# Kernel tuning notes

Measured on AMD Instinct MI355X. Metric: run time of the kernel, lower is better.

Reference implementation:

```python
import jax, jax.numpy as jnp
import numpy as np

B, C, H, W = 8, 256, 64, 64
NUM_HEADS = 4


def setup_inputs() -> dict:
    key = jax.random.key(0)
    ks = jax.random.split(key, 6)
    s = 0.02  # small init scale for 1x1 conv weights
    return {
        "x": jax.random.normal(ks[0], (B, C, H, W), jnp.float32),
        "cproj": jax.random.normal(ks[1], (B, C, H, W), jnp.float32),
        "wq": jax.random.normal(ks[2], (C, C), jnp.float32) * s,
        "bq": jnp.zeros((C,), jnp.float32),
        "wkv": jax.random.normal(ks[3], (2 * C, C), jnp.float32) * s,
        "bkv": jnp.zeros((2 * C,), jnp.float32),
        "wo": jax.random.normal(ks[4], (C, C), jnp.float32) * s,  # zero_module in torch; random here for a meaningful baseline
        "bo": jnp.zeros((C,), jnp.float32),
    }


def reference(x, cproj, wq, bq, wkv, bkv, wo, bo):
    Bb, Cc, Hh, Ww = x.shape
    N = Hh * Ww
    h = NUM_HEADS
    d = Cc // h
    scale = 1.0 / jnp.sqrt(jnp.sqrt(jnp.asarray(Cc, jnp.float32)))

    xf = x.reshape(Bb, Cc, N)
    cf = cproj.reshape(Bb, Cc, N)

    # 1x1 convs == channel matmuls
    Q = jnp.einsum('oc,bcn->bon', wq, xf) + bq[None, :, None]           # (B,C,N)
    KV = jnp.einsum('oc,bcn->bon', wkv, cf) + bkv[None, :, None]        # (B,2C,N)
    K, V = KV[:, :Cc], KV[:, Cc:]

    # softmax over channel-dim-within-head for q, over spatial N for k
    q = jax.nn.softmax(Q.reshape(Bb, h, d, N) * scale, axis=2).reshape(Bb, Cc, N)
    k = jax.nn.softmax(K.reshape(Bb, h, d, N), axis=3).reshape(Bb, Cc, N)

    # linear-attention: (B,C,C) context, then project back to N — note heads are mixed, per original bmm
    context = jnp.einsum('bcn,bdn->bcd', k, V)
    out = jnp.einsum('bcd,bdn->bcn', context, q)

    out = jnp.einsum('oc,bcn->bon', wo, out) + bo[None, :, None]
    return out.reshape(Bb, Cc, Hh, Ww)
```

## Files before the change

### kernel.cpp

```cpp
#include <hip/hip_runtime.h>

#define B_ 8
#define C_ 256
#define N_ 4096
#define H_ 4
#define KVC_ 512
#define NSPLIT 8

typedef float f32x4 __attribute__((ext_vector_type(4)));
typedef __bf16 bf16x8 __attribute__((ext_vector_type(8)));
typedef unsigned short u16x8 __attribute__((ext_vector_type(8)));
typedef unsigned short u16x4 __attribute__((ext_vector_type(4)));

union BU8 { u16x8 u; bf16x8 b; };

__device__ __forceinline__ unsigned short f2bf(float f) {
  unsigned u = __float_as_uint(f);
  u += 0x7fff + ((u >> 16) & 1);
  return (unsigned short)(u >> 16);
}

__device__ __forceinline__ f32x4 mfma16(bf16x8 a, bf16x8 b, f32x4 c) {
  return __builtin_amdgcn_mfma_f32_16x16x32_bf16(a, b, c, 0, 0, 0);
}

__global__ __launch_bounds__(256) void qproj_softmax(
    const float* __restrict__ wq, const float* __restrict__ x,
    const float* __restrict__ bq, unsigned short* __restrict__ qT) {
  __shared__ unsigned short As[256][40];
  __shared__ unsigned short Bs[32][68];
  __shared__ float bql[C_];
  const int b = blockIdx.z;
  const int n0 = blockIdx.x * 64;
  const int tid = threadIdx.x;
  const int lane = tid & 63, w = tid >> 6;
  const float* xb = x + (size_t)b * C_ * N_;

  bql[tid] = bq[tid];

  f32x4 acc[16];
#pragma unroll
  for (int i = 0; i < 16; i++) acc[i] = (f32x4){0.f, 0.f, 0.f, 0.f};

  const int colL = lane & 15, kq = lane >> 4;
  const int ra = tid >> 3, ca = (tid & 7) * 4;
  const int rb = tid >> 4, cb = (tid & 15) * 4;

  float4 pa[8], pb[2];
#pragma unroll
  for (int i = 0; i < 8; i++) pa[i] = *(const float4*)&wq[(i * 32 + ra) * C_ + ca];
#pragma unroll
  for (int i = 0; i < 2; i++) pb[i] = *(const float4*)&xb[(size_t)(i * 16 + rb) * N_ + n0 + cb];

  for (int kt = 0; kt < 8; kt++) {
#pragma unroll
    for (int i = 0; i < 8; i++) {
      float4 v = pa[i];
      *(u16x4*)&As[i * 32 + ra][ca] = (u16x4){f2bf(v.x), f2bf(v.y), f2bf(v.z), f2bf(v.w)};
    }
#pragma unroll
    for (int i = 0; i < 2; i++) {
      float4 v = pb[i];
      *(u16x4*)&Bs[i * 16 + rb][cb] = (u16x4){f2bf(v.x), f2bf(v.y), f2bf(v.z), f2bf(v.w)};
    }
    __syncthreads();
    if (kt < 7) {
      const int kc = (kt + 1) * 32;
#pragma unroll
      for (int i = 0; i < 8; i++) pa[i] = *(const float4*)&wq[(i * 32 + ra) * C_ + kc + ca];
#pragma unroll
      for (int i = 0; i < 2; i++) pb[i] = *(const float4*)&xb[(size_t)(kc + i * 16 + rb) * N_ + n0 + cb];
    }
    BU8 bu;
#pragma unroll
    for (int j = 0; j < 8; j++) bu.u[j] = Bs[kq * 8 + j][w * 16 + colL];
    bf16x8 bf = bu.b;
#pragma unroll
    for (int mt = 0; mt < 16; mt++) {
      bf16x8 af = *(const bf16x8*)&As[mt * 16 + colL][kq * 8];
      acc[mt] = mfma16(af, bf, acc[mt]);
    }
    __syncthreads();
  }

  const int quad = lane >> 4;
  const int n = n0 + w * 16 + colL;
  unsigned short* qbase = qT + ((size_t)b * N_ + n) * C_;
#pragma unroll
  for (int h = 0; h < H_; h++) {
    float v[16];
    float mx = -1e30f;
#pragma unroll
    for (int i = 0; i < 4; i++) {
      int mt = 4 * h + i;
#pragma unroll
      for (int r = 0; r < 4; r++) {
        int m = mt * 16 + quad * 4 + r;
        float val = (acc[mt][r] + bql[m]) * 0.25f;
        v[i * 4 + r] = val;
        mx = fmaxf(mx, val);
      }
    }
    mx = fmaxf(mx, __shfl_xor(mx, 16));
    mx = fmaxf(mx, __shfl_xor(mx, 32));
    float s = 0.f;
#pragma unroll
    for (int j = 0; j < 16; j++) { v[j] = __expf(v[j] - mx); s += v[j]; }
    s += __shfl_xor(s, 16);
    s += __shfl_xor(s, 32);
    float inv = 1.0f / s;
#pragma unroll
    for (int i = 0; i < 4; i++) {
      u16x4 o = (u16x4){f2bf(v[i * 4 + 0] * inv), f2bf(v[i * 4 + 1] * inv),
                        f2bf(v[i * 4 + 2] * inv), f2bf(v[i * 4 + 3] * inv)};
      *(u16x4*)(qbase + (4 * h + i) * 16 + quad * 4) = o;
    }
  }
}

__global__ __launch_bounds__(256) void kvproj(
    const float* __restrict__ wkv, const float* __restrict__ cp,
    const float* __restrict__ bkv, float* __restrict__ Kf,
    unsigned short* __restrict__ Vb) {
  __shared__ unsigned short As[128][40];
  __shared__ unsigned short Bs[32][136];
  const int b = blockIdx.z;
  const int m0 = blockIdx.y * 128, n0 = blockIdx.x * 128;
  const int tid = threadIdx.x, lane = tid & 63, w = tid >> 6;
  const int m0w = (w >> 1) * 64, n0w = (w & 1) * 64;
  const int colL = lane & 15, kq = lane >> 4;
  const float* cpb = cp + (size_t)b * C_ * N_;

  f32x4 acc[4][4];
#pragma unroll
  for (int i = 0; i < 4; i++)
#pragma unroll
    for (int j = 0; j < 4; j++) acc[i][j] = (f32x4){0.f, 0.f, 0.f, 0.f};

  const int ra = tid >> 3, ca = (tid & 7) * 4;
  const int rb = tid >> 5, cb = (tid & 31) * 4;

  float4 pa[4], pb[4];
#pragma unroll
  for (int i = 0; i < 4; i++) pa[i] = *(const float4*)&wkv[(size_t)(m0 + i * 32 + ra) * C_ + ca];
#pragma unroll
  for (int i = 0; i < 4; i++) pb[i] = *(const float4*)&cpb[(size_t)(i * 8 + rb) * N_ + n0 + cb];

  for (int kt = 0; kt < 8; kt++) {
#pragma unroll
    for (int i = 0; i < 4; i++) {
      float4 v = pa[i];
      *(u16x4*)&As[i * 32 + ra][ca] = (u16x4){f2bf(v.x), f2bf(v.y), f2bf(v.z), f2bf(v.w)};
    }
#pragma unroll
    for (int i = 0; i < 4; i++) {
      float4 v = pb[i];
      *(u16x4*)&Bs[i * 8 + rb][cb] = (u16x4){f2bf(v.x), f2bf(v.y), f2bf(v.z), f2bf(v.w)};
    }
    __syncthreads();
    if (kt < 7) {
      const int kc = (kt + 1) * 32;
#pragma unroll
      for (int i = 0; i < 4; i++) pa[i] = *(const float4*)&wkv[(size_t)(m0 + i * 32 + ra) * C_ + kc + ca];
#pragma unroll
      for (int i = 0; i < 4; i++) pb[i] = *(const float4*)&cpb[(size_t)(kc + i * 8 + rb) * N_ + n0 + cb];
    }
    bf16x8 bfr[4];
#pragma unroll
    for (int nt = 0; nt < 4; nt++) {
      BU8 bu;
#pragma unroll
      for (int j = 0; j < 8; j++) bu.u[j] = Bs[kq * 8 + j][n0w + nt * 16 + colL];
      bfr[nt] = bu.b;
    }
#pragma unroll
    for (int mt = 0; mt < 4; mt++) {
      bf16x8 af = *(const bf16x8*)&As[m0w + mt * 16 + colL][kq * 8];
#pragma unroll
      for (int nt = 0; nt < 4; nt++) acc[mt][nt] = mfma16(af, bfr[nt], acc[mt][nt]);
    }
    __syncthreads();
  }

  const int quad = lane >> 4;
#pragma unroll
  for (int mt = 0; mt < 4; mt++) {
#pragma unroll
    for (int r = 0; r < 4; r++) {
      int m = m0 + m0w + mt * 16 + quad * 4 + r;
      float bias = bkv[m];
#pragma unroll
      for (int nt = 0; nt < 4; nt++) {
        int n = n0 + n0w + nt * 16 + colL;
        float val = acc[mt][nt][r] + bias;
        if (m0 < C_) {
          Kf[((size_t)b * C_ + m) * N_ + n] = val;
        } else {
          Vb[((size_t)b * C_ + (m - C_)) * N_ + n] = f2bf(val);
        }
      }
    }
  }
}

__global__ __launch_bounds__(256) void ksoftmax(const float* __restrict__ Kf,
                                                unsigned short* __restrict__ kb) {
  const int b = blockIdx.x >> 8, c = blockIdx.x & 255;
  const float* row = Kf + ((size_t)b * C_ + c) * N_;
  unsigned short* orow = kb + ((size_t)b * C_ + c) * N_;
  const int t = threadIdx.x, lane = t & 63, wv = t >> 6;
  __shared__ float red[8];

  float4 v[4];
  float mx = -1e30f;
#pragma unroll
  for (int i = 0; i < 4; i++) {
    v[i] = *(const float4*)&row[i * 1024 + t * 4];
    mx = fmaxf(fmaxf(fmaxf(mx, v[i].x), fmaxf(v[i].y, v[i].z)), v[i].w);
  }
#pragma unroll
  for (int o = 32; o > 0; o >>= 1) mx = fmaxf(mx, __shfl_down(mx, o));
  if (lane == 0) red[wv] = mx;
  __syncthreads();
  mx = fmaxf(fmaxf(red[0], red[1]), fmaxf(red[2], red[3]));

  float s = 0.f;
#pragma unroll
  for (int i = 0; i < 4; i++) {
    v[i].x = __expf(v[i].x - mx); v[i].y = __expf(v[i].y - mx);
    v[i].z = __expf(v[i].z - mx); v[i].w = __expf(v[i].w - mx);
    s += v[i].x + v[i].y + v[i].z + v[i].w;
  }
#pragma unroll
  for (int o = 32; o > 0; o >>= 1) s += __shfl_down(s, o);
  if (lane == 0) red[4 + wv] = s;
  __syncthreads();
  float inv = 1.0f / (red[4] + red[5] + red[6] + red[7]);
#pragma unroll
  for (int i = 0; i < 4; i++) {
    u16x4 o = (u16x4){f2bf(v[i].x * inv), f2bf(v[i].y * inv),
                      f2bf(v[i].z * inv), f2bf(v[i].w * inv)};
    *(u16x4*)&orow[i * 1024 + t * 4] = o;
  }
}

__global__ __launch_bounds__(256) void ctx_part(
    const unsigned short* __restrict__ kb, const unsigned short* __restrict__ Vb,
    float* __restrict__ ctxp) {
  __shared__ unsigned short As[128][72];
  __shared__ unsigned short Bs[128][72];
  const int z = blockIdx.z, b = z >> 3, s = z & 7;
  const int m0 = blockIdx.y * 128, n0 = blockIdx.x * 128;
  const int tid = threadIdx.x, lane = tid & 63, w = tid >> 6;
  const int m0w = (w >> 1) * 64, n0w = (w & 1) * 64;
  const int colL = lane & 15, kq = lane >> 4;
  const unsigned short* Ab = kb + (size_t)b * C_ * N_;
  const unsigned short* Bb = Vb + (size_t)b * C_ * N_;

  f32x4 acc[4][4];
#pragma unroll
  for (int i = 0; i < 4; i++)
#pragma unroll
    for (int j = 0; j < 4; j++) acc[i][j] = (f32x4){0.f, 0.f, 0.f, 0.f};

  const int rs = tid >> 3, cs = (tid & 7) * 8;
  const int kbeg = s * (N_ / NSPLIT);

  u16x8 pa[4], pb[4];
#pragma unroll
  for (int i = 0; i < 4; i++) {
    pa[i] = *(const u16x8*)&Ab[(size_t)(m0 + i * 32 + rs) * N_ + kbeg + cs];
    pb[i] = *(const u16x8*)&Bb[(size_t)(n0 + i * 32 + rs) * N_ + kbeg + cs];
  }

  for (int kt = 0; kt < (N_ / NSPLIT) / 64; kt++) {
#pragma unroll
    for (int i = 0; i < 4; i++) {
      *(u16x8*)&As[i * 32 + rs][cs] = pa[i];
      *(u16x8*)&Bs[i * 32 + rs][cs] = pb[i];
    }
    __syncthreads();
    if (kt < (N_ / NSPLIT) / 64 - 1) {
      const int kc = kbeg + (kt + 1) * 64;
#pragma unroll
      for (int i = 0; i < 4; i++) {
        pa[i] = *(const u16x8*)&Ab[(size_t)(m0 + i * 32 + rs) * N_ + kc + cs];
        pb[i] = *(const u16x8*)&Bb[(size_t)(n0 + i * 32 + rs) * N_ + kc + cs];
      }
    }
#pragma unroll
    for (int ks = 0; ks < 2; ks++) {
      bf16x8 af[4], bfr[4];
#pragma unroll
      for (int mt = 0; mt < 4; mt++) af[mt] = *(const bf16x8*)&As[m0w + mt * 16 + colL][ks * 32 + kq * 8];
#pragma unroll
      for (int nt = 0; nt < 4; nt++) bfr[nt] = *(const bf16x8*)&Bs[n0w + nt * 16 + colL][ks * 32 + kq * 8];
#pragma unroll
      for (int mt = 0; mt < 4; mt++)
#pragma unroll
        for (int nt = 0; nt < 4; nt++) acc[mt][nt] = mfma16(af[mt], bfr[nt], acc[mt][nt]);
    }
    __syncthreads();
  }

  float* outp = ctxp + ((size_t)s * B_ + b) * C_ * C_;
  const int quad = lane >> 4;
#pragma unroll
  for (int mt = 0; mt < 4; mt++)
#pragma unroll
    for (int nt = 0; nt < 4; nt++)
#pragma unroll
      for (int r = 0; r < 4; r++) {
        int m = m0 + m0w + mt * 16 + quad * 4 + r;
        int n = n0 + n0w + nt * 16 + colL;
        outp[(size_t)m * C_ + n] = acc[mt][nt][r];
      }
}

__global__ __launch_bounds__(256) void ctx_reduce(const float* __restrict__ ctxp,
                                                  unsigned short* __restrict__ ctxs) {
  const size_t e = ((size_t)blockIdx.x * 256 + threadIdx.x) * 4;
  float4 a = {0.f, 0.f, 0.f, 0.f};
#pragma unroll
  for (int s = 0; s < NSPLIT; s++) {
    float4 v = *(const float4*)&ctxp[(size_t)s * B_ * C_ * C_ + e];
    a.x += v.x; a.y += v.y; a.z += v.z; a.w += v.w;
  }
  *(u16x4*)&ctxs[e] = (u16x4){f2bf(a.x), f2bf(a.y), f2bf(a.z), f2bf(a.w)};
}

__global__ __launch_bounds__(256) void oproj(const float* __restrict__ wo,
                                             const unsigned short* __restrict__ ctxs,
                                             unsigned short* __restrict__ ctx2) {
  __shared__ unsigned short As[128][40];
  __shared__ unsigned short Bs[32][136];
  const int b = blockIdx.z;
  const int m0 = blockIdx.y * 128, n0 = blockIdx.x * 128;
  const int tid = threadIdx.x, lane = tid & 63, w = tid >> 6;
  const int m0w = (w >> 1) * 64, n0w = (w & 1) * 64;
  const int colL = lane & 15, kq = lane >> 4;
  const unsigned short* cb = ctxs + (size_t)b * C_ * C_;

  f32x4 acc[4][4];
#pragma unroll
  for (int i = 0; i < 4; i++)
#pragma unroll
    for (int j = 0; j < 4; j++) acc[i][j] = (f32x4){0.f, 0.f, 0.f, 0.f};

  for (int kc = 0; kc < C_; kc += 32) {
    __syncthreads();
#pragma unroll
    for (int i = 0; i < 4; i++) {
      int r = i * 32 + (tid >> 3), c = (tid & 7) * 4;
      float4 v = *(const float4*)&wo[(size_t)(m0 + r) * C_ + kc + c];
      *(u16x4*)&As[r][c] = (u16x4){f2bf(v.x), f2bf(v.y), f2bf(v.z), f2bf(v.w)};
    }
#pragma unroll
    for (int i = 0; i < 2; i++) {
      int r = i * 16 + (tid >> 4), c = (tid & 15) * 8;
      *(u16x8*)&Bs[r][c] = *(const u16x8*)&cb[(size_t)(kc + r) * C_ + n0 + c];
    }
    __syncthreads();

    bf16x8 bfr[4];
#pragma unroll
    for (int nt = 0; nt < 4; nt++) {
      BU8 bu;
#pragma unroll
      for (int j = 0; j < 8; j++) bu.u[j] = Bs[kq * 8 + j][n0w + nt * 16 + colL];
      bfr[nt] = bu.b;
    }
#pragma unroll
    for (int mt = 0; mt < 4; mt++) {
      bf16x8 af = *(const bf16x8*)&As[m0w + mt * 16 + colL][kq * 8];
#pragma unroll
      for (int nt = 0; nt < 4; nt++) acc[mt][nt] = mfma16(af, bfr[nt], acc[mt][nt]);
    }
  }

  unsigned short* ob = ctx2 + (size_t)b * C_ * C_;
  const int quad = lane >> 4;
#pragma unroll
  for (int mt = 0; mt < 4; mt++)
#pragma unroll
    for (int nt = 0; nt < 4; nt++)
#pragma unroll
      for (int r = 0; r < 4; r++) {
        int m = m0 + m0w + mt * 16 + quad * 4 + r;
        int n = n0 + n0w + nt * 16 + colL;
        ob[(size_t)m * C_ + n] = f2bf(acc[mt][nt][r]);
      }
}

__global__ __launch_bounds__(256) void outgemm(const unsigned short* __restrict__ ctx2,
                                               const unsigned short* __restrict__ qT,
                                               const float* __restrict__ bo,
                                               float* __restrict__ out) {
  __shared__ unsigned short As[128][72];
  __shared__ unsigned short Bs[128][72];
  const int b = blockIdx.z;
  const int n0 = blockIdx.x * 128, m0 = blockIdx.y * 128;
  const int tid = threadIdx.x, lane = tid & 63, w = tid >> 6;
  const int m0w = (w >> 1) * 64, n0w = (w & 1) * 64;
  const int colL = lane & 15, kq = lane >> 4;
  const unsigned short* Ab = ctx2 + (size_t)b * C_ * C_;
  const unsigned short* Bb = qT + (size_t)b * N_ * C_;

  f32x4 acc[4][4];
#pragma unroll
  for (int i = 0; i < 4; i++)
#pragma unroll
    for (int j = 0; j < 4; j++) acc[i][j] = (f32x4){0.f, 0.f, 0.f, 0.f};

  const int rs = tid >> 3, cs = (tid & 7) * 8;

  u16x8 pa[4], pb[4];
#pragma unroll
  for (int i = 0; i < 4; i++) {
    pa[i] = *(const u16x8*)&Ab[(size_t)(m0 + i * 32 + rs) * C_ + cs];
    pb[i] = *(const u16x8*)&Bb[(size_t)(n0 + i * 32 + rs) * C_ + cs];
  }

  for (int kt = 0; kt < 4; kt++) {
#pragma unroll
    for (int i = 0; i < 4; i++) {
      *(u16x8*)&As[i * 32 + rs][cs] = pa[i];
      *(u16x8*)&Bs[i * 32 + rs][cs] = pb[i];
    }
    __syncthreads();
    if (kt < 3) {
      const int kc = (kt + 1) * 64;
#pragma unroll
      for (int i = 0; i < 4; i++) {
        pa[i] = *(const u16x8*)&Ab[(size_t)(m0 + i * 32 + rs) * C_ + kc + cs];
        pb[i] = *(const u16x8*)&Bb[(size_t)(n0 + i * 32 + rs) * C_ + kc + cs];
      }
    }
#pragma unroll
    for (int ks = 0; ks < 2; ks++) {
      bf16x8 af[4], bfr[4];
#pragma unroll
      for (int mt = 0; mt < 4; mt++) af[mt] = *(const bf16x8*)&As[m0w + mt * 16 + colL][ks * 32 + kq * 8];
#pragma unroll
      for (int nt = 0; nt < 4; nt++) bfr[nt] = *(const bf16x8*)&Bs[n0w + nt * 16 + colL][ks * 32 + kq * 8];
#pragma unroll
      for (int mt = 0; mt < 4; mt++)
#pragma unroll
        for (int nt = 0; nt < 4; nt++) acc[mt][nt] = mfma16(af[mt], bfr[nt], acc[mt][nt]);
    }
    __syncthreads();
  }

  float* ob = out + (size_t)b * C_ * N_;
  const int quad = lane >> 4;
#pragma unroll
  for (int mt = 0; mt < 4; mt++)
#pragma unroll
    for (int r = 0; r < 4; r++) {
      int m = m0 + m0w + mt * 16 + quad * 4 + r;
      float bias = bo[m];
#pragma unroll
      for (int nt = 0; nt < 4; nt++) {
        int n = n0 + n0w + nt * 16 + colL;
        ob[(size_t)m * N_ + n] = acc[mt][nt][r] + bias;
      }
    }
}

extern "C" void kernel_launch(void* const* d_in, const int* in_sizes, int n_in,
                              void* d_out, int out_size, void* d_ws, size_t ws_size,
                              hipStream_t stream) {
  const float* x     = (const float*)d_in[0];
  const float* cproj = (const float*)d_in[1];
  const float* wq    = (const float*)d_in[2];
  const float* bq    = (const float*)d_in[3];
  const float* wkv   = (const float*)d_in[4];
  const float* bkv   = (const float*)d_in[5];
  const float* wo    = (const float*)d_in[6];
  const float* bo    = (const float*)d_in[7];
  float* out = (float*)d_out;

  unsigned short* qT   = (unsigned short*)d_ws;
  float*          Kf   = (float*)(qT + (size_t)B_ * N_ * C_);
  unsigned short* Vb   = (unsigned short*)(Kf + (size_t)B_ * C_ * N_);
  unsigned short* kb   = Vb + (size_t)B_ * C_ * N_;
  float*          ctxp = (float*)(kb + (size_t)B_ * C_ * N_);
  unsigned short* ctxs = (unsigned short*)(ctxp + (size_t)NSPLIT * B_ * C_ * C_);
  unsigned short* ctx2 = ctxs + (size_t)B_ * C_ * C_;

  qproj_softmax<<<dim3(N_ / 64, 1, B_), 256, 0, stream>>>(wq, x, bq, qT);
  kvproj<<<dim3(N_ / 128, KVC_ / 128, B_), 256, 0, stream>>>(wkv, cproj, bkv, Kf, Vb);
  ksoftmax<<<dim3(B_ * C_), 256, 0, stream>>>(Kf, kb);
  ctx_part<<<dim3(2, 2, B_ * NSPLIT), 256, 0, stream>>>(kb, Vb, ctxp);
  ctx_reduce<<<dim3(B_ * C_ * C_ / 1024), 256, 0, stream>>>(ctxp, ctxs);
  oproj<<<dim3(2, 2, B_), 256, 0, stream>>>(wo, ctxs, ctx2);
  outgemm<<<dim3(N_ / 128, 2, B_), 256, 0, stream>>>(ctx2, qT, bo, out);
}
```

Measured before the change: 207.7 us.

## Store B tiles transposed in LDS for vector fragment loads; halve ctx tile width

```diff
diff --git a/kernel.cpp b/kernel.cpp
--- a/kernel.cpp
+++ b/kernel.cpp
@@ -12,13 +12,14 @@
 typedef unsigned short u16x8 __attribute__((ext_vector_type(8)));
 typedef unsigned short u16x4 __attribute__((ext_vector_type(4)));
 
-union BU8 { u16x8 u; bf16x8 b; };
-
 __device__ __forceinline__ unsigned short f2bf(float f) {
   unsigned u = __float_as_uint(f);
   u += 0x7fff + ((u >> 16) & 1);
   return (unsigned short)(u >> 16);
 }
+__device__ __forceinline__ unsigned pack2(float lo, float hi) {
+  return (unsigned)f2bf(lo) | ((unsigned)f2bf(hi) << 16);
+}
 
 __device__ __forceinline__ f32x4 mfma16(bf16x8 a, bf16x8 b, f32x4 c) {
   return __builtin_amdgcn_mfma_f32_16x16x32_bf16(a, b, c, 0, 0, 0);
@@ -28,7 +29,7 @@
     const float* __restrict__ wq, const float* __restrict__ x,
     const float* __restrict__ bq, unsigned short* __restrict__ qT) {
   __shared__ unsigned short As[256][40];
-  __shared__ unsigned short Bs[32][68];
+  __shared__ unsigned short Bs[64][40];
   __shared__ float bql[C_];
   const int b = blockIdx.z;
   const int n0 = blockIdx.x * 64;
@@ -44,13 +45,13 @@
 
   const int colL = lane & 15, kq = lane >> 4;
   const int ra = tid >> 3, ca = (tid & 7) * 4;
-  const int rb = tid >> 4, cb = (tid & 15) * 4;
-
-  float4 pa[8], pb[2];
+  const int kp = tid >> 4, nf = tid & 15;
+
+  float4 pa[8], pb0, pb1;
 #pragma unroll
   for (int i = 0; i < 8; i++) pa[i] = *(const float4*)&wq[(i * 32 + ra) * C_ + ca];
-#pragma unroll
-  for (int i = 0; i < 2; i++) pb[i] = *(const float4*)&xb[(size_t)(i * 16 + rb) * N_ + n0 + cb];
+  pb0 = *(const float4*)&xb[(size_t)(2 * kp) * N_ + n0 + 4 * nf];
+  pb1 = *(const float4*)&xb[(size_t)(2 * kp + 1) * N_ + n0 + 4 * nf];
 
   for (int kt = 0; kt < 8; kt++) {
 #pragma unroll
@@ -58,23 +59,22 @@
       float4 v = pa[i];
       *(u16x4*)&As[i * 32 + ra][ca] = (u16x4){f2bf(v.x), f2bf(v.y), f2bf(v.z), f2bf(v.w)};
     }
-#pragma unroll
-    for (int i = 0; i < 2; i++) {
-      float4 v = pb[i];
-      *(u16x4*)&Bs[i * 16 + rb][cb] = (u16x4){f2bf(v.x), f2bf(v.y), f2bf(v.z), f2bf(v.w)};
+    {
+      const float* q0 = (const float*)&pb0;
+      const float* q1 = (const float*)&pb1;
+#pragma unroll
+      for (int j = 0; j < 4; j++)
+        *(unsigned*)&Bs[4 * nf + j][2 * kp] = pack2(q0[j], q1[j]);
     }
     __syncthreads();
     if (kt < 7) {
       const int kc = (kt + 1) * 32;
 #pragma unroll
       for (int i = 0; i < 8; i++) pa[i] = *(const float4*)&wq[(i * 32 + ra) * C_ + kc + ca];
-#pragma unroll
-      for (int i = 0; i < 2; i++) pb[i] = *(const float4*)&xb[(size_t)(kc + i * 16 + rb) * N_ + n0 + cb];
-    }
-    BU8 bu;
-#pragma unroll
-    for (int j = 0; j < 8; j++) bu.u[j] = Bs[kq * 8 + j][w * 16 + colL];
-    bf16x8 bf = bu.b;
+      pb0 = *(const float4*)&xb[(size_t)(kc + 2 * kp) * N_ + n0 + 4 * nf];
+      pb1 = *(const float4*)&xb[(size_t)(kc + 2 * kp + 1) * N_ + n0 + 4 * nf];
+    }
+    bf16x8 bf = *(const bf16x8*)&Bs[w * 16 + colL][kq * 8];
 #pragma unroll
     for (int mt = 0; mt < 16; mt++) {
       bf16x8 af = *(const bf16x8*)&As[mt * 16 + colL][kq * 8];
@@ -123,7 +123,7 @@
     const float* __restrict__ bkv, float* __restrict__ Kf,
     unsigned short* __restrict__ Vb) {
   __shared__ unsigned short As[128][40];
-  __shared__ unsigned short Bs[32][136];
+  __shared__ unsigned short Bs[128][40];
   const int b = blockIdx.z;
   const int m0 = blockIdx.y * 128, n0 = blockIdx.x * 128;
   const int tid = threadIdx.x, lane = tid & 63, w = tid >> 6;
@@ -138,13 +138,16 @@
     for (int j = 0; j < 4; j++) acc[i][j] = (f32x4){0.f, 0.f, 0.f, 0.f};
 
   const int ra = tid >> 3, ca = (tid & 7) * 4;
-  const int rb = tid >> 5, cb = (tid & 31) * 4;
-
-  float4 pa[4], pb[4];
+  const int kp = tid >> 4, nf2 = tid & 15;
+
+  float4 pa[4], pb[2][2];
 #pragma unroll
   for (int i = 0; i < 4; i++) pa[i] = *(const float4*)&wkv[(size_t)(m0 + i * 32 + ra) * C_ + ca];
 #pragma unroll
-  for (int i = 0; i < 4; i++) pb[i] = *(const float4*)&cpb[(size_t)(i * 8 + rb) * N_ + n0 + cb];
+  for (int i = 0; i < 2; i++) {
+    pb[i][0] = *(const float4*)&cpb[(size_t)(2 * kp) * N_ + n0 + 4 * nf2 + 64 * i];
+    pb[i][1] = *(const float4*)&cpb[(size_t)(2 * kp + 1) * N_ + n0 + 4 * nf2 + 64 * i];
+  }
 
   for (int kt = 0; kt < 8; kt++) {
 #pragma unroll
@@ -153,9 +156,12 @@
       *(u16x4*)&As[i * 32 + ra][ca] = (u16x4){f2bf(v.x), f2bf(v.y), f2bf(v.z), f2bf(v.w)};
     }
 #pragma unroll
-    for (int i = 0; i < 4; i++) {
-      float4 v = pb[i];
-      *(u16x4*)&Bs[i * 8 + rb][cb] = (u16x4){f2bf(v.x), f2bf(v.y), f2bf(v.z), f2bf(v.w)};
+    for (int i = 0; i < 2; i++) {
+      const float* q0 = (const float*)&pb[i][0];
+      const float* q1 = (const float*)&pb[i][1];
+#pragma unroll
+      for (int j = 0; j < 4; j++)
+        *(unsigned*)&Bs[4 * nf2 + 64 * i + j][2 * kp] = pack2(q0[j], q1[j]);
     }
     __syncthreads();
     if (kt < 7) {
@@ -163,16 +169,14 @@
 #pragma unroll
       for (int i = 0; i < 4; i++) pa[i] = *(const float4*)&wkv[(size_t)(m0 + i * 32 + ra) * C_ + kc + ca];
 #pragma unroll
-      for (int i = 0; i < 4; i++) pb[i] = *(const float4*)&cpb[(size_t)(kc + i * 8 + rb) * N_ + n0 + cb];
+      for (int i = 0; i < 2; i++) {
+        pb[i][0] = *(const float4*)&cpb[(size_t)(kc + 2 * kp) * N_ + n0 + 4 * nf2 + 64 * i];
+        pb[i][1] = *(const float4*)&cpb[(size_t)(kc + 2 * kp + 1) * N_ + n0 + 4 * nf2 + 64 * i];
+      }
     }
     bf16x8 bfr[4];
 #pragma unroll
-    for (int nt = 0; nt < 4; nt++) {
-      BU8 bu;
-#pragma unroll
-      for (int j = 0; j < 8; j++) bu.u[j] = Bs[kq * 8 + j][n0w + nt * 16 + colL];
-      bfr[nt] = bu.b;
-    }
+    for (int nt = 0; nt < 4; nt++) bfr[nt] = *(const bf16x8*)&Bs[n0w + nt * 16 + colL][kq * 8];
 #pragma unroll
     for (int mt = 0; mt < 4; mt++) {
       bf16x8 af = *(const bf16x8*)&As[m0w + mt * 16 + colL][kq * 8];
@@ -248,57 +252,54 @@
     const unsigned short* __restrict__ kb, const unsigned short* __restrict__ Vb,
     float* __restrict__ ctxp) {
   __shared__ unsigned short As[128][72];
-  __shared__ unsigned short Bs[128][72];
+  __shared__ unsigned short Bs[64][72];
   const int z = blockIdx.z, b = z >> 3, s = z & 7;
-  const int m0 = blockIdx.y * 128, n0 = blockIdx.x * 128;
+  const int m0 = blockIdx.y * 128, n0 = blockIdx.x * 64;
   const int tid = threadIdx.x, lane = tid & 63, w = tid >> 6;
-  const int m0w = (w >> 1) * 64, n0w = (w & 1) * 64;
+  const int m0w = (w & 1) * 64, n0w = (w >> 1) * 32;
   const int colL = lane & 15, kq = lane >> 4;
   const unsigned short* Ab = kb + (size_t)b * C_ * N_;
   const unsigned short* Bb = Vb + (size_t)b * C_ * N_;
 
-  f32x4 acc[4][4];
+  f32x4 acc[4][2];
 #pragma unroll
   for (int i = 0; i < 4; i++)
 #pragma unroll
-    for (int j = 0; j < 4; j++) acc[i][j] = (f32x4){0.f, 0.f, 0.f, 0.f};
+    for (int j = 0; j < 2; j++) acc[i][j] = (f32x4){0.f, 0.f, 0.f, 0.f};
 
   const int rs = tid >> 3, cs = (tid & 7) * 8;
   const int kbeg = s * (N_ / NSPLIT);
 
-  u16x8 pa[4], pb[4];
-#pragma unroll
-  for (int i = 0; i < 4; i++) {
-    pa[i] = *(const u16x8*)&Ab[(size_t)(m0 + i * 32 + rs) * N_ + kbeg + cs];
-    pb[i] = *(const u16x8*)&Bb[(size_t)(n0 + i * 32 + rs) * N_ + kbeg + cs];
-  }
+  u16x8 pa[4], pb[2];
+#pragma unroll
+  for (int i = 0; i < 4; i++) pa[i] = *(const u16x8*)&Ab[(size_t)(m0 + i * 32 + rs) * N_ + kbeg + cs];
+#pragma unroll
+  for (int i = 0; i < 2; i++) pb[i] = *(const u16x8*)&Bb[(size_t)(n0 + i * 32 + rs) * N_ + kbeg + cs];
 
   for (int kt = 0; kt < (N_ / NSPLIT) / 64; kt++) {
 #pragma unroll
-    for (int i = 0; i < 4; i++) {
-      *(u16x8*)&As[i * 32 + rs][cs] = pa[i];
-      *(u16x8*)&Bs[i * 32 + rs][cs] = pb[i];
-    }
+    for (int i = 0; i < 4; i++) *(u16x8*)&As[i * 32 + rs][cs] = pa[i];
+#pragma unroll
+    for (int i = 0; i < 2; i++) *(u16x8*)&Bs[i * 32 + rs][cs] = pb[i];
     __syncthreads();
     if (kt < (N_ / NSPLIT) / 64 - 1) {
       const int kc = kbeg + (kt + 1) * 64;
 #pragma unroll
-      for (int i = 0; i < 4; i++) {
-        pa[i] = *(const u16x8*)&Ab[(size_t)(m0 + i * 32 + rs) * N_ + kc + cs];
-        pb[i] = *(const u16x8*)&Bb[(size_t)(n0 + i * 32 + rs) * N_ + kc + cs];
-      }
+      for (int i = 0; i < 4; i++) pa[i] = *(const u16x8*)&Ab[(size_t)(m0 + i * 32 + rs) * N_ + kc + cs];
+#pragma unroll
+      for (int i = 0; i < 2; i++) pb[i] = *(const u16x8*)&Bb[(size_t)(n0 + i * 32 + rs) * N_ + kc + cs];
     }
 #pragma unroll
     for (int ks = 0; ks < 2; ks++) {
-      bf16x8 af[4], bfr[4];
+      bf16x8 af[4], bfr[2];
 #pragma unroll
       for (int mt = 0; mt < 4; mt++) af[mt] = *(const bf16x8*)&As[m0w + mt * 16 + colL][ks * 32 + kq * 8];
 #pragma unroll
-      for (int nt = 0; nt < 4; nt++) bfr[nt] = *(const bf16x8*)&Bs[n0w + nt * 16 + colL][ks * 32 + kq * 8];
+      for (int nt = 0; nt < 2; nt++) bfr[nt] = *(const bf16x8*)&Bs[n0w + nt * 16 + colL][ks * 32 + kq * 8];
 #pragma unroll
       for (int mt = 0; mt < 4; mt++)
 #pragma unroll
-        for (int nt = 0; nt < 4; nt++) acc[mt][nt] = mfma16(af[mt], bfr[nt], acc[mt][nt]);
+        for (int nt = 0; nt < 2; nt++) acc[mt][nt] = mfma16(af[mt], bfr[nt], acc[mt][nt]);
     }
     __syncthreads();
   }
@@ -308,7 +309,7 @@
 #pragma unroll
   for (int mt = 0; mt < 4; mt++)
 #pragma unroll
-    for (int nt = 0; nt < 4; nt++)
+    for (int nt = 0; nt < 2; nt++)
 #pragma unroll
       for (int r = 0; r < 4; r++) {
         int m = m0 + m0w + mt * 16 + quad * 4 + r;
@@ -333,7 +334,7 @@
                                              const unsigned short* __restrict__ ctxs,
                                              unsigned short* __restrict__ ctx2) {
   __shared__ unsigned short As[128][40];
-  __shared__ unsigned short Bs[32][136];
+  __shared__ unsigned short Bs[128][40];
   const int b = blockIdx.z;
   const int m0 = blockIdx.y * 128, n0 = blockIdx.x * 128;
   const int tid = threadIdx.x, lane = tid & 63, w = tid >> 6;
@@ -347,6 +348,8 @@
 #pragma unroll
     for (int j = 0; j < 4; j++) acc[i][j] = (f32x4){0.f, 0.f, 0.f, 0.f};
 
+  const int kp = tid >> 4, nf2 = tid & 15;
+
   for (int kc = 0; kc < C_; kc += 32) {
     __syncthreads();
 #pragma unroll
@@ -357,19 +360,17 @@
     }
 #pragma unroll
     for (int i = 0; i < 2; i++) {
-      int r = i * 16 + (tid >> 4), c = (tid & 15) * 8;
-      *(u16x8*)&Bs[r][c] = *(const u16x8*)&cb[(size_t)(kc + r) * C_ + n0 + c];
+      u16x4 a0 = *(const u16x4*)&cb[(size_t)(kc + 2 * kp) * C_ + n0 + 4 * nf2 + 64 * i];
+      u16x4 a1 = *(const u16x4*)&cb[(size_t)(kc + 2 * kp + 1) * C_ + n0 + 4 * nf2 + 64 * i];
+#pragma unroll
+      for (int j = 0; j < 4; j++)
+        *(unsigned*)&Bs[4 * nf2 + 64 * i + j][2 * kp] = (unsigned)a0[j] | ((unsigned)a1[j] << 16);
     }
     __syncthreads();
 
     bf16x8 bfr[4];
 #pragma unroll
-    for (int nt = 0; nt < 4; nt++) {
-      BU8 bu;
-#pragma unroll
-      for (int j = 0; j < 8; j++) bu.u[j] = Bs[kq * 8 + j][n0w + nt * 16 + colL];
-      bfr[nt] = bu.b;
-    }
+    for (int nt = 0; nt < 4; nt++) bfr[nt] = *(const bf16x8*)&Bs[n0w + nt * 16 + colL][kq * 8];
 #pragma unroll
     for (int mt = 0; mt < 4; mt++) {
       bf16x8 af = *(const bf16x8*)&As[m0w + mt * 16 + colL][kq * 8];
@@ -491,7 +492,7 @@
   qproj_softmax<<<dim3(N_ / 64, 1, B_), 256, 0, stream>>>(wq, x, bq, qT);
   kvproj<<<dim3(N_ / 128, KVC_ / 128, B_), 256, 0, stream>>>(wkv, cproj, bkv, Kf, Vb);
   ksoftmax<<<dim3(B_ * C_), 256, 0, stream>>>(Kf, kb);
-  ctx_part<<<dim3(2, 2, B_ * NSPLIT), 256, 0, stream>>>(kb, Vb, ctxp);
+  ctx_part<<<dim3(4, 2, B_ * NSPLIT), 256, 0, stream>>>(kb, Vb, ctxp);
   ctx_reduce<<<dim3(B_ * C_ * C_ / 1024), 256, 0, stream>>>(ctxp, ctxs);
   oproj<<<dim3(2, 2, B_), 256, 0, stream>>>(wo, ctxs, ctx2);
   outgemm<<<dim3(N_ / 128, 2, B_), 256, 0, stream>>>(ctx2, qT, bo, out);
```

Result: no change. 204.7 us (-1.4%).
